# Optimization experiments

Measured on AMD Instinct MI355X. Metric: run time of the kernel, lower is better.

## Reference

```python
import jax, jax.numpy as jnp
import numpy as np
import math

D_MODEL = 1024
NUM_HEADS = 16
SEQ = 2048
BATCH = 4


def setup_inputs() -> dict:
    key = jax.random.key(0)
    ks = jax.random.split(key, 7)
    s = 0.02
    return {
        "x": jax.random.normal(ks[0], (BATCH, SEQ, D_MODEL), jnp.float32),
        "Wq": jax.random.normal(ks[1], (D_MODEL, D_MODEL), jnp.float32) * s,
        "bq": jax.random.normal(ks[2], (D_MODEL,), jnp.float32) * s,
        "Wkv": jax.random.normal(ks[3], (D_MODEL, 2 * D_MODEL), jnp.float32) * s,
        "bkv": jax.random.normal(ks[4], (2 * D_MODEL,), jnp.float32) * s,
        "Wo": jax.random.normal(ks[5], (D_MODEL, D_MODEL), jnp.float32) * s,
        "bo": jax.random.normal(ks[6], (D_MODEL,), jnp.float32) * s,
        "decoderMask": 1,
    }


def reference(x, Wq, bq, Wkv, bkv, Wo, bo, decoderMask):
    B, S, D = x.shape
    H = NUM_HEADS
    dh = D // H
    q_ = x @ Wq + bq              # [B,S,D]
    kv_ = x @ Wkv + bkv           # [B,S,2D] (self-attention: m is None)
    # Faithful to source: concat [q_, kv_] then reshape into heads of 3*dh,
    # which interleaves Q/KV projection columns across heads.
    qkv = jnp.concatenate([q_, kv_], axis=-1)          # [B,S,3D]
    qkv = qkv.reshape(B, S, H, 3 * dh).transpose(0, 2, 1, 3)  # [B,H,S,3dh]
    q, k, v = jnp.split(qkv, 3, axis=-1)               # each [B,H,S,dh]
    scaled = jnp.einsum("bhqd,bhkd->bhqk", q, k) / math.sqrt(dh)
    if decoderMask:
        mask = jnp.triu(jnp.full((S, S), -jnp.inf, dtype=scaled.dtype), k=1)
        scaled = scaled + mask
    attn = jax.nn.softmax(scaled, axis=-1)
    vals = jnp.einsum("bhqk,bhkd->bhqd", attn, v)      # [B,H,S,dh]
    vals = vals.transpose(0, 2, 1, 3).reshape(B, S, D)
    return vals @ Wo + bo
```

## Files before the change

kernel.cpp:

```cpp
#include <hip/hip_runtime.h>
#include <cstddef>
#include <cstdint>

#define SEQ   2048
#define BATCH 4
#define DM    1024
#define NH    16
#define DH    64
#define ROWS  (BATCH*SEQ)
#define NC3   3072
#define SM_SCALE 0.18033688f

typedef unsigned short u16;
typedef __attribute__((ext_vector_type(8))) short bf16x8;
typedef __attribute__((ext_vector_type(2))) float f32x2;
typedef __attribute__((ext_vector_type(4))) float f32x4;
typedef __attribute__((ext_vector_type(16))) float f32x16;
typedef __attribute__((ext_vector_type(4))) unsigned u32x4;
typedef __attribute__((ext_vector_type(2))) unsigned u32x2;

union V16 { f32x16 v; f32x2 p[8]; };

__device__ __forceinline__ u16 f2b(float f) {
  union { float f; unsigned u; } v; v.f = f;
  unsigned r = v.u + 0x7fffu + ((v.u >> 16) & 1u);
  return (u16)(r >> 16);
}

__device__ __forceinline__ unsigned cvt_pk_bf16(float lo, float hi) {
  unsigned r;
  asm("v_cvt_pk_bf16_f32 %0, %1, %2" : "=v"(r) : "v"(lo), "v"(hi));
  return r;
}

__device__ __forceinline__ void plswap(unsigned& a, unsigned& b) {
  auto rr = __builtin_amdgcn_permlane32_swap((int)a, (int)b, false, false);
  a = (unsigned)rr[0];
  b = (unsigned)rr[1];
}

__device__ __forceinline__ float ex2(float x) { return __builtin_amdgcn_exp2f(x); }

__device__ __forceinline__ void gld16(const void* g, void* l) {
  __builtin_amdgcn_global_load_lds((const __attribute__((address_space(1))) void*)g,
                                   (__attribute__((address_space(3))) void*)l,
                                   16, 0, 0);
}

__global__ __launch_bounds__(256) void prep_tw_kernel(
    const float* __restrict__ x, const float* __restrict__ bq,
    const float* __restrict__ bkv, u16* __restrict__ xb, float* __restrict__ bc,
    const float* __restrict__ Wq, const float* __restrict__ Wkv,
    const float* __restrict__ Wo, u16* __restrict__ Wt)
{
  __shared__ float t_[32][33];
  const int tid = threadIdx.x;
  if (blockIdx.x < 8192) {
    int i = blockIdx.x * 256 + tid;
    int idx = i * 4;
    float4 v = *(const float4*)(x + idx);
    xb[idx + 0] = f2b(v.x);
    xb[idx + 1] = f2b(v.y);
    xb[idx + 2] = f2b(v.z);
    xb[idx + 3] = f2b(v.w);
    if (i < NC3) bc[i] = (i < DM) ? bq[i] : bkv[i - DM];
  } else {
    const int bid = blockIdx.x - 8192;
    const int n0 = (bid & 127) * 32, k0 = (bid >> 7) * 32;
    const int xcol = tid & 31, yrow = tid >> 5;
    #pragma unroll
    for (int it = 0; it < 4; ++it) {
      int k = k0 + yrow + it * 8;
      int n = n0 + xcol;
      float v;
      if (n < DM)           v = Wq[k * DM + n];
      else if (n < NC3)     v = Wkv[k * (2 * DM) + (n - DM)];
      else                  v = Wo[k * DM + (n - NC3)];
      t_[yrow + it * 8][xcol] = v;
    }
    __syncthreads();
    #pragma unroll
    for (int it = 0; it < 4; ++it) {
      int n = n0 + yrow + it * 8;
      int k = k0 + xcol;
      Wt[(size_t)n * DM + k] = f2b(t_[xcol][yrow + it * 8]);
    }
  }
}

template <int MODE>
__global__ __launch_bounds__(256) void gemm_bt(
    const u16* __restrict__ A, const u16* __restrict__ Bt,
    const float* __restrict__ bias, void* __restrict__ C,
    u16* __restrict__ Vt, int M, int N, int K)
{
  __shared__ alignas(16) u16 lds_[3 * 8192];
  const int tid = threadIdx.x;
  const int lane = tid & 63, wid = tid >> 6;
  const int wr = (wid >> 1) * 64, wc = (wid & 1) * 64;
  const int l15 = lane & 15, lhi = lane >> 4;

  const int bid = blockIdx.x;
  const int xcd = bid & 7, t = bid >> 3;
  const int rsub = t & 7, colb = t >> 3;
  const int row0 = (xcd * 8 + rsub) * 128, col0 = colb * 128;
  const int sr = tid >> 2, scol = (tid & 3) * 8;

  const u16* aS0 = A  + (size_t)(row0 + sr) * K + scol;
  const u16* aS1 = A  + (size_t)(row0 + 64 + sr) * K + scol;
  const u16* bS0 = Bt + (size_t)(col0 + sr) * K + scol;
  const u16* bS1 = Bt + (size_t)(col0 + 64 + sr) * K + scol;
  const int dA = tid * 8;

  int aoff[4], boff[4];
  #pragma unroll
  for (int m = 0; m < 4; ++m) aoff[m] = (wr + m * 16 + l15) * 32 + lhi * 8;
  #pragma unroll
  for (int n = 0; n < 4; ++n) boff[n] = 4096 + (wc + n * 16 + l15) * 32 + lhi * 8;

  f32x4 acc[4][4];
  #pragma unroll
  for (int m = 0; m < 4; ++m)
    #pragma unroll
    for (int n = 0; n < 4; ++n) { f32x4 z = {0.f, 0.f, 0.f, 0.f}; acc[m][n] = z; }

  const int KT = K >> 5;

  auto stage = [&](int kt, u16* base) {
    const int ka = kt * 32;
    gld16(aS0 + ka, base + dA);
    gld16(aS1 + ka, base + 2048 + dA);
    gld16(bS0 + ka, base + 4096 + dA);
    gld16(bS1 + ka, base + 6144 + dA);
  };

  u16* const bufA = lds_;
  u16* const bufB = lds_ + 8192;
  u16* const bufC = lds_ + 16384;

  stage(0, bufA); stage(1, bufB);
  asm volatile("s_waitcnt vmcnt(4)" ::: "memory");
  __builtin_amdgcn_s_barrier();

  u16* rb = bufA;
  u16* sb = bufC;
  for (int kt = 0; kt < KT; ++kt) {
    bf16x8 a[4], b[4];
    #pragma unroll
    for (int m = 0; m < 4; ++m) a[m] = *(const bf16x8*)&rb[aoff[m]];
    #pragma unroll
    for (int n = 0; n < 4; ++n) b[n] = *(const bf16x8*)&rb[boff[n]];
    if (kt + 2 < KT) stage(kt + 2, sb);
    __builtin_amdgcn_s_setprio(1);
    #pragma unroll
    for (int m = 0; m < 4; ++m)
      #pragma unroll
      for (int n = 0; n < 4; ++n)
        acc[m][n] = __builtin_amdgcn_mfma_f32_16x16x32_bf16(a[m], b[n], acc[m][n], 0, 0, 0);
    __builtin_amdgcn_s_setprio(0);
    if (kt + 1 < KT) {
      if (kt + 2 < KT) { asm volatile("s_waitcnt vmcnt(4)" ::: "memory"); }
      else             { asm volatile("s_waitcnt vmcnt(0)" ::: "memory"); }
      __builtin_amdgcn_s_barrier();
    }
    rb = (rb == bufC) ? bufA : rb + 8192;
    sb = (sb == bufC) ? bufA : sb + 8192;
  }

  #pragma unroll
  for (int m = 0; m < 4; ++m)
    #pragma unroll
    for (int n = 0; n < 4; ++n) {
      const int col = col0 + wc + n * 16 + l15;
      const float bv = bias[col];
      if (MODE == 0) {
        #pragma unroll
        for (int r = 0; r < 4; ++r) {
          const int row = row0 + wr + m * 16 + lhi * 4 + r;
          ((float*)C)[(size_t)row * N + col] = acc[m][n][r] + bv;
        }
      } else {
        const int hh = col / 192;
        const int cc = col - hh * 192;
        if (cc < 128) {
          const float qs = (cc < 64) ? SM_SCALE : 1.f;
          #pragma unroll
          for (int r = 0; r < 4; ++r) {
            const int row = row0 + wr + m * 16 + lhi * 4 + r;
            ((u16*)C)[(size_t)row * N + col] = f2b((acc[m][n][r] + bv) * qs);
          }
        } else {
          u16 wv[4];
          #pragma unroll
          for (int r = 0; r < 4; ++r) wv[r] = f2b(acc[m][n][r] + bv);
          const int row = row0 + wr + m * 16 + lhi * 4;
          const int bb = row >> 11, j = row & (SEQ - 1);
          u16* vt = Vt + ((size_t)(bb * NH + hh) * 64 + (cc - 128)) * SEQ + j;
          u32x2 pv = { (unsigned)wv[0] | ((unsigned)wv[1] << 16),
                       (unsigned)wv[2] | ((unsigned)wv[3] << 16) };
          *(u32x2*)vt = pv;
        }
      }
    }
}

__global__ __launch_bounds__(256) void attn_kernel(
    const u16* __restrict__ qkv, const u16* __restrict__ Vt, u16* __restrict__ ctx)
{
  const int bid = blockIdx.x;
  const int p   = (bid >> 3) & 7;
  const int g   = (bid & 7) + ((bid >> 6) << 3);
  const int h   = g & 15, b = g >> 4;
  const int tid = threadIdx.x;
  const int lane = tid & 63, wid = tid >> 6;
  const int l31 = lane & 31, lhi5 = lane >> 5;

  __shared__ alignas(16) u16 smem[4 * 64 * 64];

  const size_t kv_row = (size_t)(b * NH + h) * 64;
  const int sr = tid >> 3, sck = tid & 7;
  const int scks = sck ^ (sr & 7);

  const u16* kSrc0 = qkv + (size_t)(b * SEQ + sr) * NC3 + h * 192 + 64 + scks * 8;
  const u16* kSrc1 = kSrc0 + (size_t)32 * NC3;
  const u16* vSrc0 = Vt + (kv_row + sr) * SEQ + scks * 8;
  const u16* vSrc1 = vSrc0 + (size_t)32 * SEQ;
  const int dOff0 = sr * 64 + sck * 8;
  const int dOff1 = (32 + sr) * 64 + sck * 8;

  int koff[4], koff2[4];
  #pragma unroll
  for (int c = 0; c < 4; ++c) {
    koff[c]  = l31 * 64        + (((2 * c + lhi5) ^ (l31 & 7)) * 8);
    koff2[c] = (32 + l31) * 64 + (((2 * c + lhi5) ^ (l31 & 7)) * 8);
  }

  #pragma unroll 1
  for (int half = 0; half < 2; ++half) {
    const int qt = half ? (7 - p) : (8 + p);
    const int q0 = qt * 128;

    #pragma unroll
    for (int it = 0; it < 4; ++it) {
      int row = it * 32 + sr;
      gld16(qkv + (size_t)(b * SEQ + q0 + row) * NC3 + h * 192 + scks * 8,
            &smem[row * 64 + sck * 8]);
    }
    gld16(kSrc0, &smem[8192 + dOff0]);
    gld16(kSrc1, &smem[8192 + dOff1]);
    gld16(vSrc0, &smem[12288 + dOff0]);
    gld16(vSrc1, &smem[12288 + dOff1]);
    __syncthreads();

    bf16x8 qf[4];
    {
      const int qrow = wid * 32 + l31;
      #pragma unroll
      for (int c = 0; c < 4; ++c)
        qf[c] = *(const bf16x8*)&smem[qrow * 64 + (((2 * c + lhi5) ^ (qrow & 7)) * 8)];
    }
    __syncthreads();

    V16 o0, o1;
    #pragma unroll
    for (int r = 0; r < 16; ++r) { o0.v[r] = 0.f; o1.v[r] = 0.f; }
    float lrow = 0.f;

    const int nt = qt * 2 + 2;
    const int qw0 = q0 + wid * 32;
    const int qa  = qw0 + l31;
    const int dqb = qa - 4 * lhi5;

    for (int jt = 0; jt < nt; ++jt) {
      const int j0 = jt * 64;
      const u16* Kb = smem + ((jt & 1) ? 0 : 8192);
      const u16* Vb = smem + ((jt & 1) ? 4096 : 12288);

      if (jt + 1 < nt) {
        u16* Kn = smem + ((jt & 1) ? 8192 : 0);
        u16* Vn = smem + ((jt & 1) ? 12288 : 4096);
        const size_t kAdv = (size_t)(j0 + 64) * NC3;
        const int    vAdv = j0 + 64;
        gld16(kSrc0 + kAdv, &Kn[dOff0]);
        gld16(kSrc1 + kAdv, &Kn[dOff1]);
        gld16(vSrc0 + vAdv, &Vn[dOff0]);
        gld16(vSrc1 + vAdv, &Vn[dOff1]);
      }

      if (j0 <= qw0 + 31) {
        V16 s0, s1;
        #pragma unroll
        for (int r = 0; r < 16; ++r) { s0.v[r] = 0.f; s1.v[r] = 0.f; }
        __builtin_amdgcn_s_setprio(1);
        #pragma unroll
        for (int c = 0; c < 4; ++c) {
          bf16x8 kf = *(const bf16x8*)&Kb[koff[c]];
          s0.v = __builtin_amdgcn_mfma_f32_32x32x16_bf16(kf, qf[c], s0.v, 0, 0, 0);
        }
        #pragma unroll
        for (int c = 0; c < 4; ++c) {
          bf16x8 kf = *(const bf16x8*)&Kb[koff2[c]];
          s1.v = __builtin_amdgcn_mfma_f32_32x32x16_bf16(kf, qf[c], s1.v, 0, 0, 0);
        }
        __builtin_amdgcn_s_setprio(0);

        if (j0 + 63 > qw0) {
          const int dq = dqb - j0;
          #pragma unroll
          for (int r = 0; r < 16; ++r) {
            const int kvc = (r & 3) + 8 * (r >> 2);
            s0.v[r] = (kvc > dq)      ? -1e30f : s0.v[r];
            s1.v[r] = (kvc + 32 > dq) ? -1e30f : s1.v[r];
          }
        }

        f32x2 sum2 = {0.f, 0.f};
        #pragma unroll
        for (int i = 0; i < 8; ++i) {
          f32x2 e0, e1;
          e0[0] = ex2(s0.p[i][0]); e0[1] = ex2(s0.p[i][1]);
          e1[0] = ex2(s1.p[i][0]); e1[1] = ex2(s1.p[i][1]);
          s0.p[i] = e0; s1.p[i] = e1;
          sum2 += e0 + e1;
        }
        float ps = sum2[0] + sum2[1];
        {
          unsigned a = __builtin_bit_cast(unsigned, ps), bb = a;
          plswap(a, bb);
          ps = __builtin_bit_cast(float, a) + __builtin_bit_cast(float, bb);
        }
        lrow += ps;

        unsigned pk0[8], pk1[8];
        #pragma unroll
        for (int i = 0; i < 4; ++i) {
          pk0[2 * i]     = cvt_pk_bf16(s0.v[4 * i + 0], s0.v[4 * i + 1]);
          pk0[2 * i + 1] = cvt_pk_bf16(s0.v[4 * i + 2], s0.v[4 * i + 3]);
          pk1[2 * i]     = cvt_pk_bf16(s1.v[4 * i + 0], s1.v[4 * i + 1]);
          pk1[2 * i + 1] = cvt_pk_bf16(s1.v[4 * i + 2], s1.v[4 * i + 3]);
        }
        bf16x8 pf[4];
        {
          unsigned a0 = pk0[0], b0 = pk0[2]; plswap(a0, b0);
          unsigned a1 = pk0[1], b1 = pk0[3]; plswap(a1, b1);
          u32x4 w0v = {a0, a1, b0, b1}; pf[0] = __builtin_bit_cast(bf16x8, w0v);
          unsigned a2 = pk0[4], b2 = pk0[6]; plswap(a2, b2);
          unsigned a3 = pk0[5], b3 = pk0[7]; plswap(a3, b3);
          u32x4 w1v = {a2, a3, b2, b3}; pf[1] = __builtin_bit_cast(bf16x8, w1v);
          unsigned a4 = pk1[0], b4 = pk1[2]; plswap(a4, b4);
          unsigned a5 = pk1[1], b5 = pk1[3]; plswap(a5, b5);
          u32x4 w2v = {a4, a5, b4, b5}; pf[2] = __builtin_bit_cast(bf16x8, w2v);
          unsigned a6 = pk1[4], b6 = pk1[6]; plswap(a6, b6);
          unsigned a7 = pk1[5], b7 = pk1[7]; plswap(a7, b7);
          u32x4 w3v = {a6, a7, b6, b7}; pf[3] = __builtin_bit_cast(bf16x8, w3v);
        }

        __builtin_amdgcn_s_setprio(1);
        #pragma unroll
        for (int c = 0; c < 4; ++c) {
          bf16x8 vf = *(const bf16x8*)&Vb[koff[c]];
          o0.v = __builtin_amdgcn_mfma_f32_32x32x16_bf16(vf, pf[c], o0.v, 0, 0, 0);
        }
        #pragma unroll
        for (int c = 0; c < 4; ++c) {
          bf16x8 vf = *(const bf16x8*)&Vb[koff2[c]];
          o1.v = __builtin_amdgcn_mfma_f32_32x32x16_bf16(vf, pf[c], o1.v, 0, 0, 0);
        }
        __builtin_amdgcn_s_setprio(0);
      }
      __syncthreads();
    }

    const float inv = 1.f / lrow;
    u16* crow = ctx + (size_t)(b * SEQ + qa) * DM + h * DH;
    #pragma unroll
    for (int i = 0; i < 4; ++i) {
      u32x2 v0, v1;
      v0[0] = cvt_pk_bf16(o0.v[4 * i + 0] * inv, o0.v[4 * i + 1] * inv);
      v0[1] = cvt_pk_bf16(o0.v[4 * i + 2] * inv, o0.v[4 * i + 3] * inv);
      v1[0] = cvt_pk_bf16(o1.v[4 * i + 0] * inv, o1.v[4 * i + 1] * inv);
      v1[1] = cvt_pk_bf16(o1.v[4 * i + 2] * inv, o1.v[4 * i + 3] * inv);
      *(u32x2*)&crow[8 * i + 4 * lhi5]      = v0;
      *(u32x2*)&crow[32 + 8 * i + 4 * lhi5] = v1;
    }
  }
}

extern "C" void kernel_launch(void* const* d_in, const int* in_sizes, int n_in,
                              void* d_out, int out_size, void* d_ws, size_t ws_size,
                              hipStream_t stream) {
  (void)in_sizes; (void)n_in; (void)out_size; (void)ws_size;
  const float* x   = (const float*)d_in[0];
  const float* Wq  = (const float*)d_in[1];
  const float* bq  = (const float*)d_in[2];
  const float* Wkv = (const float*)d_in[3];
  const float* bkv = (const float*)d_in[4];
  const float* Wo  = (const float*)d_in[5];
  const float* bo  = (const float*)d_in[6];
  float* out = (float*)d_out;

  char* w = (char*)d_ws;
  size_t off = 0;
  auto alloc = [&](size_t bytes) { void* p = w + off; off += (bytes + 255) & ~(size_t)255; return p; };
  u16*   xb   = (u16*)alloc((size_t)ROWS * DM * 2);
  u16*   qkvb = (u16*)alloc((size_t)ROWS * NC3 * 2);
  u16*   Vt   = (u16*)alloc((size_t)BATCH * NH * DH * SEQ * 2);
  u16*   Wt   = (u16*)alloc((size_t)4096 * DM * 2);
  float* bc   = (float*)alloc((size_t)NC3 * 4);
  u16*   ctx  = xb;

  prep_tw_kernel<<<dim3(8192 + 4096), 256, 0, stream>>>(x, bq, bkv, xb, bc, Wq, Wkv, Wo, Wt);
  gemm_bt<1><<<dim3((ROWS / 128) * (NC3 / 128)), 256, 0, stream>>>(xb, Wt, bc, qkvb, Vt, ROWS, NC3, DM);
  attn_kernel<<<dim3(512), 256, 0, stream>>>(qkvb, Vt, ctx);
  gemm_bt<0><<<dim3((ROWS / 128) * (DM / 128)), 256, 0, stream>>>(ctx, Wt + (size_t)NC3 * DM, bo, out, nullptr, ROWS, DM, DM);
}
```

Baseline: 161.6 us.

## Triple-buffer K/V tiles in attention with prefetch distance two

Replaces the double-buffered K/V shared-memory pipeline with a three-slot ring, issuing loads two tiles ahead and using explicit vmcnt waits plus raw barriers instead of __syncthreads. Q gets a dedicated LDS region, so the extra barrier after reading Q fragments is removed. The aim is to hide global-load latency behind more compute. In exchange, LDS per block grows from 32KB to 64KB, which may reduce occupancy, and the hand-counted vmcnt values must match the number of outstanding loads exactly.

```diff
diff --git a/kernel.cpp b/kernel.cpp
--- a/kernel.cpp
+++ b/kernel.cpp
@@ -215,16 +215,20 @@
   const int lane = tid & 63, wid = tid >> 6;
   const int l31 = lane & 31, lhi5 = lane >> 5;
 
-  __shared__ alignas(16) u16 smem[4 * 64 * 64];
+  __shared__ alignas(16) u16 smem[8192 + 3 * 8192];
+  u16* const Qs = smem;
+  u16* const R0 = smem + 8192;
+  u16* const R1 = R0 + 8192;
+  u16* const R2 = R1 + 8192;
 
   const size_t kv_row = (size_t)(b * NH + h) * 64;
   const int sr = tid >> 3, sck = tid & 7;
   const int scks = sck ^ (sr & 7);
 
-  const u16* kSrc0 = qkv + (size_t)(b * SEQ + sr) * NC3 + h * 192 + 64 + scks * 8;
-  const u16* kSrc1 = kSrc0 + (size_t)32 * NC3;
-  const u16* vSrc0 = Vt + (kv_row + sr) * SEQ + scks * 8;
-  const u16* vSrc1 = vSrc0 + (size_t)32 * SEQ;
+  const u16* kBase = qkv + (size_t)(b * SEQ + sr) * NC3 + h * 192 + 64 + scks * 8;
+  const u16* vBase = Vt + (kv_row + sr) * SEQ + scks * 8;
+  const size_t kRow32 = (size_t)32 * NC3;
+  const size_t vRow32 = (size_t)32 * SEQ;
   const int dOff0 = sr * 64 + sck * 8;
   const int dOff1 = (32 + sr) * 64 + sck * 8;
 
@@ -239,55 +243,57 @@
   for (int half = 0; half < 2; ++half) {
     const int qt = half ? (7 - p) : (8 + p);
     const int q0 = qt * 128;
+    const int nt = qt * 2 + 2;
 
     #pragma unroll
     for (int it = 0; it < 4; ++it) {
       int row = it * 32 + sr;
       gld16(qkv + (size_t)(b * SEQ + q0 + row) * NC3 + h * 192 + scks * 8,
-            &smem[row * 64 + sck * 8]);
-    }
-    gld16(kSrc0, &smem[8192 + dOff0]);
-    gld16(kSrc1, &smem[8192 + dOff1]);
-    gld16(vSrc0, &smem[12288 + dOff0]);
-    gld16(vSrc1, &smem[12288 + dOff1]);
-    __syncthreads();
+            Qs + row * 64 + sck * 8);
+    }
+    {
+      const u16* ks = kBase;          const u16* vs = vBase;
+      gld16(ks,          R0 + dOff0); gld16(ks + kRow32, R0 + dOff1);
+      gld16(vs,          R0 + 4096 + dOff0); gld16(vs + vRow32, R0 + 4096 + dOff1);
+      ks = kBase + (size_t)64 * NC3;  vs = vBase + 64;
+      gld16(ks,          R1 + dOff0); gld16(ks + kRow32, R1 + dOff1);
+      gld16(vs,          R1 + 4096 + dOff0); gld16(vs + vRow32, R1 + 4096 + dOff1);
+    }
+    asm volatile("s_waitcnt vmcnt(4)" ::: "memory");
+    __builtin_amdgcn_s_barrier();
 
     bf16x8 qf[4];
     {
       const int qrow = wid * 32 + l31;
       #pragma unroll
       for (int c = 0; c < 4; ++c)
-        qf[c] = *(const bf16x8*)&smem[qrow * 64 + (((2 * c + lhi5) ^ (qrow & 7)) * 8)];
-    }
-    __syncthreads();
+        qf[c] = *(const bf16x8*)&Qs[qrow * 64 + (((2 * c + lhi5) ^ (qrow & 7)) * 8)];
+    }
 
     V16 o0, o1;
     #pragma unroll
     for (int r = 0; r < 16; ++r) { o0.v[r] = 0.f; o1.v[r] = 0.f; }
     float lrow = 0.f;
 
-    const int nt = qt * 2 + 2;
     const int qw0 = q0 + wid * 32;
     const int qa  = qw0 + l31;
     const int dqb = qa - 4 * lhi5;
 
+    u16* rb = R0;
+    u16* sb = R2;
     for (int jt = 0; jt < nt; ++jt) {
       const int j0 = jt * 64;
-      const u16* Kb = smem + ((jt & 1) ? 0 : 8192);
-      const u16* Vb = smem + ((jt & 1) ? 4096 : 12288);
-
-      if (jt + 1 < nt) {
-        u16* Kn = smem + ((jt & 1) ? 8192 : 0);
-        u16* Vn = smem + ((jt & 1) ? 12288 : 4096);
-        const size_t kAdv = (size_t)(j0 + 64) * NC3;
-        const int    vAdv = j0 + 64;
-        gld16(kSrc0 + kAdv, &Kn[dOff0]);
-        gld16(kSrc1 + kAdv, &Kn[dOff1]);
-        gld16(vSrc0 + vAdv, &Vn[dOff0]);
-        gld16(vSrc1 + vAdv, &Vn[dOff1]);
+
+      if (jt + 2 < nt) {
+        const u16* ks = kBase + (size_t)(j0 + 128) * NC3;
+        const u16* vs = vBase + (j0 + 128);
+        gld16(ks,          sb + dOff0); gld16(ks + kRow32, sb + dOff1);
+        gld16(vs,          sb + 4096 + dOff0); gld16(vs + vRow32, sb + 4096 + dOff1);
       }
 
       if (j0 <= qw0 + 31) {
+        const u16* Kb = rb;
+        const u16* Vb = rb + 4096;
         V16 s0, s1;
         #pragma unroll
         for (int r = 0; r < 16; ++r) { s0.v[r] = 0.f; s1.v[r] = 0.f; }
@@ -368,7 +374,12 @@
         }
         __builtin_amdgcn_s_setprio(0);
       }
-      __syncthreads();
+
+      if (jt + 2 < nt)      { asm volatile("s_waitcnt vmcnt(4)" ::: "memory"); }
+      else if (jt + 1 < nt) { asm volatile("s_waitcnt vmcnt(0)" ::: "memory"); }
+      __builtin_amdgcn_s_barrier();
+      rb = (rb == R2) ? R0 : rb + 8192;
+      sb = (sb == R2) ? R0 : sb + 8192;
     }
 
     const float inv = 1.f / lrow;
```

After: 162.3 us. About the same (+0.4%).

## Rewrite projection GEMMs with 256x128 tiles, 8 waves, and swizzled LDS

Applied to the files above, without the earlier changes.

Replaces the 128x128, 4-wave GEMM with a 256x128 tile kernel using 512 threads, a K-step of 64 with XOR-swizzled LDS layout, and a finer-grained staging schedule that interleaves global loads with MFMA phases. The larger tile is meant to raise operand reuse per LDS load and to cut bank conflicts, while the phased prefetch aims to hide memory latency. In exchange it uses 96KB of LDS per block and adds more barriers per K-step, and the grid becomes 768 and 256 blocks, which may leave some CUs idle.

```diff
diff --git a/kernel.cpp b/kernel.cpp
--- a/kernel.cpp
+++ b/kernel.cpp
@@ -88,35 +88,47 @@
   }
 }
 
-template <int MODE>
-__global__ __launch_bounds__(256) void gemm_bt(
+template <int MODE, int N, int NCOLB>
+__global__ __launch_bounds__(512, 2) void gemm4(
     const u16* __restrict__ A, const u16* __restrict__ Bt,
-    const float* __restrict__ bias, void* __restrict__ C,
-    u16* __restrict__ Vt, int M, int N, int K)
+    const float* __restrict__ bias, void* __restrict__ C, u16* __restrict__ Vt)
 {
-  __shared__ alignas(16) u16 lds_[3 * 8192];
+  constexpr int K = 1024;
+  constexpr int ASLOT = 16384;
+  constexpr int BBASE = 32768;
+  constexpr int BSLOT = 8192;
+  __shared__ alignas(16) u16 lds_[49152];
+
   const int tid = threadIdx.x;
   const int lane = tid & 63, wid = tid >> 6;
-  const int wr = (wid >> 1) * 64, wc = (wid & 1) * 64;
+  const int wr4 = wid >> 1, wc2 = wid & 1;
   const int l15 = lane & 15, lhi = lane >> 4;
 
   const int bid = blockIdx.x;
   const int xcd = bid & 7, t = bid >> 3;
-  const int rsub = t & 7, colb = t >> 3;
-  const int row0 = (xcd * 8 + rsub) * 128, col0 = colb * 128;
-  const int sr = tid >> 2, scol = (tid & 3) * 8;
-
-  const u16* aS0 = A  + (size_t)(row0 + sr) * K + scol;
-  const u16* aS1 = A  + (size_t)(row0 + 64 + sr) * K + scol;
-  const u16* bS0 = Bt + (size_t)(col0 + sr) * K + scol;
-  const u16* bS1 = Bt + (size_t)(col0 + 64 + sr) * K + scol;
-  const int dA = tid * 8;
-
-  int aoff[4], boff[4];
-  #pragma unroll
-  for (int m = 0; m < 4; ++m) aoff[m] = (wr + m * 16 + l15) * 32 + lhi * 8;
-  #pragma unroll
-  for (int n = 0; n < 4; ++n) boff[n] = 4096 + (wc + n * 16 + l15) * 32 + lhi * 8;
+  const int row0 = (xcd * 4 + (t & 3)) * 256;
+  const int col0 = (t >> 2) * 128;
+
+  const int sr = tid >> 3;
+  const int scg = ((tid & 7) ^ (sr & 7)) * 8;
+  const u16* aSrc = A  + (size_t)(row0 + sr) * K + scg;
+  const u16* bSrc = Bt + (size_t)(col0 + sr) * K + scg;
+  const int dLin = tid * 8;
+
+  auto stA = [&](int kt, int u) {
+    gld16(aSrc + (size_t)(u * 64) * K + kt * 64,
+          lds_ + (kt & 1) * ASLOT + u * 4096 + dLin);
+  };
+  auto stB = [&](int kt, int u) {
+    gld16(bSrc + (size_t)(u * 64) * K + kt * 64,
+          lds_ + BBASE + (kt & 1) * BSLOT + u * 4096 + dLin);
+  };
+
+  int csw[2];
+  csw[0] = ((lhi)     ^ (l15 & 7)) * 8;
+  csw[1] = ((4 + lhi) ^ (l15 & 7)) * 8;
+  const int aBase = wr4 * 4096 + l15 * 64;
+  const int bBase = BBASE + wc2 * 4096 + l15 * 64;
 
   f32x4 acc[4][4];
   #pragma unroll
@@ -124,84 +136,100 @@
     #pragma unroll
     for (int n = 0; n < 4; ++n) { f32x4 z = {0.f, 0.f, 0.f, 0.f}; acc[m][n] = z; }
 
-  const int KT = K >> 5;
-
-  auto stage = [&](int kt, u16* base) {
-    const int ka = kt * 32;
-    gld16(aS0 + ka, base + dA);
-    gld16(aS1 + ka, base + 2048 + dA);
-    gld16(bS0 + ka, base + 4096 + dA);
-    gld16(bS1 + ka, base + 6144 + dA);
-  };
-
-  u16* const bufA = lds_;
-  u16* const bufB = lds_ + 8192;
-  u16* const bufC = lds_ + 16384;
-
-  stage(0, bufA); stage(1, bufB);
-  asm volatile("s_waitcnt vmcnt(4)" ::: "memory");
+  stA(0, 0); stA(0, 1); stA(0, 2); stA(0, 3);
+  stB(0, 0); stB(0, 1);
+  stB(1, 0); stB(1, 1);
+  asm volatile("s_waitcnt vmcnt(2)" ::: "memory");
   __builtin_amdgcn_s_barrier();
 
-  u16* rb = bufA;
-  u16* sb = bufC;
-  for (int kt = 0; kt < KT; ++kt) {
-    bf16x8 a[4], b[4];
-    #pragma unroll
-    for (int m = 0; m < 4; ++m) a[m] = *(const bf16x8*)&rb[aoff[m]];
-    #pragma unroll
-    for (int n = 0; n < 4; ++n) b[n] = *(const bf16x8*)&rb[boff[n]];
-    if (kt + 2 < KT) stage(kt + 2, sb);
-    __builtin_amdgcn_s_setprio(1);
-    #pragma unroll
-    for (int m = 0; m < 4; ++m)
+  constexpr int KT2 = K / 128;
+  for (int j = 0; j < KT2; ++j) {
+    const bool last = (j == KT2 - 1);
+    #pragma unroll
+    for (int hk = 0; hk < 2; ++hk) {
+      const int aSlot = hk * ASLOT;
+      const int bSlot = hk * BSLOT;
+      bf16x8 bfr[4][2];
       #pragma unroll
-      for (int n = 0; n < 4; ++n)
-        acc[m][n] = __builtin_amdgcn_mfma_f32_16x16x32_bf16(a[m], b[n], acc[m][n], 0, 0, 0);
-    __builtin_amdgcn_s_setprio(0);
-    if (kt + 1 < KT) {
-      if (kt + 2 < KT) { asm volatile("s_waitcnt vmcnt(4)" ::: "memory"); }
-      else             { asm volatile("s_waitcnt vmcnt(0)" ::: "memory"); }
-      __builtin_amdgcn_s_barrier();
-    }
-    rb = (rb == bufC) ? bufA : rb + 8192;
-    sb = (sb == bufC) ? bufA : sb + 8192;
+      for (int ph2 = 0; ph2 < 2; ++ph2) {
+        const int gp = hk * 2 + ph2;
+        if (ph2 == 0) {
+          #pragma unroll
+          for (int n = 0; n < 4; ++n)
+            #pragma unroll
+            for (int kk = 0; kk < 2; ++kk)
+              bfr[n][kk] = *(const bf16x8*)&lds_[bBase + bSlot + n * 1024 + csw[kk]];
+        }
+        bf16x8 af[2][2];
+        #pragma unroll
+        for (int mi = 0; mi < 2; ++mi)
+          #pragma unroll
+          for (int kk = 0; kk < 2; ++kk)
+            af[mi][kk] = *(const bf16x8*)&lds_[aBase + aSlot + (ph2 * 2 + mi) * 1024 + csw[kk]];
+        switch (gp) {
+          case 0: stA(2 * j + 1, 0); stA(2 * j + 1, 1); stA(2 * j + 1, 2); break;
+          case 1: stA(2 * j + 1, 3);
+                  if (!last) { stB(2 * j + 2, 0); stB(2 * j + 2, 1); } break;
+          case 2: if (!last) { stA(2 * j + 2, 0); stA(2 * j + 2, 1); stA(2 * j + 2, 2); } break;
+          case 3: if (!last) { stA(2 * j + 2, 3); stB(2 * j + 3, 0); stB(2 * j + 3, 1); } break;
+        }
+        __builtin_amdgcn_s_barrier();
+        asm volatile("s_waitcnt lgkmcnt(0)" ::: "memory");
+        __builtin_amdgcn_sched_barrier(0);
+        __builtin_amdgcn_s_setprio(1);
+        #pragma unroll
+        for (int mi = 0; mi < 2; ++mi)
+          #pragma unroll
+          for (int n = 0; n < 4; ++n) {
+            acc[ph2 * 2 + mi][n] =
+                __builtin_amdgcn_mfma_f32_16x16x32_bf16(af[mi][0], bfr[n][0], acc[ph2 * 2 + mi][n], 0, 0, 0);
+            acc[ph2 * 2 + mi][n] =
+                __builtin_amdgcn_mfma_f32_16x16x32_bf16(af[mi][1], bfr[n][1], acc[ph2 * 2 + mi][n], 0, 0, 0);
+          }
+        __builtin_amdgcn_s_setprio(0);
+        if (gp == 1) {
+          if (last) { asm volatile("s_waitcnt vmcnt(0)" ::: "memory"); }
+          else      { asm volatile("s_waitcnt vmcnt(2)" ::: "memory"); }
+        } else if (gp == 3 && !last) {
+          asm volatile("s_waitcnt vmcnt(2)" ::: "memory");
+        }
+        __builtin_amdgcn_s_barrier();
+      }
+    }
   }
 
   #pragma unroll
-  for (int m = 0; m < 4; ++m)
+  for (int m = 0; m < 4; ++m) {
+    const int row = row0 + wr4 * 64 + m * 16 + lhi * 4;
     #pragma unroll
     for (int n = 0; n < 4; ++n) {
-      const int col = col0 + wc + n * 16 + l15;
+      const int col = col0 + wc2 * 64 + n * 16 + l15;
       const float bv = bias[col];
       if (MODE == 0) {
         #pragma unroll
-        for (int r = 0; r < 4; ++r) {
-          const int row = row0 + wr + m * 16 + lhi * 4 + r;
-          ((float*)C)[(size_t)row * N + col] = acc[m][n][r] + bv;
-        }
+        for (int r = 0; r < 4; ++r)
+          ((float*)C)[(size_t)(row + r) * N + col] = acc[m][n][r] + bv;
       } else {
         const int hh = col / 192;
         const int cc = col - hh * 192;
         if (cc < 128) {
           const float qs = (cc < 64) ? SM_SCALE : 1.f;
           #pragma unroll
-          for (int r = 0; r < 4; ++r) {
-            const int row = row0 + wr + m * 16 + lhi * 4 + r;
-            ((u16*)C)[(size_t)row * N + col] = f2b((acc[m][n][r] + bv) * qs);
-          }
+          for (int r = 0; r < 4; ++r)
+            ((u16*)C)[(size_t)(row + r) * N + col] = f2b((acc[m][n][r] + bv) * qs);
         } else {
           u16 wv[4];
           #pragma unroll
           for (int r = 0; r < 4; ++r) wv[r] = f2b(acc[m][n][r] + bv);
-          const int row = row0 + wr + m * 16 + lhi * 4;
-          const int bb = row >> 11, j = row & (SEQ - 1);
-          u16* vt = Vt + ((size_t)(bb * NH + hh) * 64 + (cc - 128)) * SEQ + j;
+          const int bb = row >> 11, jj = row & (SEQ - 1);
+          u16* vt = Vt + ((size_t)(bb * NH + hh) * 64 + (cc - 128)) * SEQ + jj;
           u32x2 pv = { (unsigned)wv[0] | ((unsigned)wv[1] << 16),
                        (unsigned)wv[2] | ((unsigned)wv[3] << 16) };
           *(u32x2*)vt = pv;
         }
       }
     }
+  }
 }
 
 __global__ __launch_bounds__(256) void attn_kernel(
@@ -410,7 +438,7 @@
   u16*   ctx  = xb;
 
   prep_tw_kernel<<<dim3(8192 + 4096), 256, 0, stream>>>(x, bq, bkv, xb, bc, Wq, Wkv, Wo, Wt);
-  gemm_bt<1><<<dim3((ROWS / 128) * (NC3 / 128)), 256, 0, stream>>>(xb, Wt, bc, qkvb, Vt, ROWS, NC3, DM);
+  gemm4<1, NC3, 24><<<dim3(768), 512, 0, stream>>>(xb, Wt, bc, qkvb, Vt);
   attn_kernel<<<dim3(512), 256, 0, stream>>>(qkvb, Vt, ctx);
-  gemm_bt<0><<<dim3((ROWS / 128) * (DM / 128)), 256, 0, stream>>>(ctx, Wt + (size_t)NC3 * DM, bo, out, nullptr, ROWS, DM, DM);
-}
+  gemm4<0, DM, 8><<<dim3(256), 512, 0, stream>>>(ctx, Wt + (size_t)NC3 * DM, bo, out, nullptr);
+}
```

Measured after the change: 160.6 us. No clear change (-0.6%).
